# Performance work log

Measured on AMD Instinct MI355X. Metric: run time of the kernel, lower is better.

Reference implementation:

```python
import jax, jax.numpy as jnp
import numpy as np

NUM_HEADS = 4
NUM_POINTS = 8


def setup_inputs() -> dict:
    key0 = jax.random.key(0)
    ks = jax.random.split(key0, 14)
    B, S, N, D, C = 1, 6, 10000, 4, 128
    Hf, Wf = 46, 80
    M = Hf * Wf
    HP2 = NUM_HEADS * NUM_POINTS * 2
    HP = NUM_HEADS * NUM_POINTS
    inp = {
        "query": jax.random.normal(ks[0], (B, N, C), jnp.float32),
        "key": jax.random.normal(ks[1], (S, M, B, C), jnp.float32),
        "value": jax.random.normal(ks[2], (S, M, B, C), jnp.float32),
        "query_pos": jax.random.normal(ks[3], (B, N, C), jnp.float32),
        "reference_points_cam": jax.random.uniform(ks[4], (S, B, N, D, 2), jnp.float32),
        "Wv": jax.random.normal(ks[5], (C, C), jnp.float32) * 0.02,
        "bv": jnp.zeros((C,), jnp.float32),
        "Wo": jax.random.normal(ks[6], (C, HP2), jnp.float32) * 0.02,
        "bo": jax.random.normal(ks[7], (HP2,), jnp.float32) * 0.5,
        "Wa": jax.random.normal(ks[8], (C, HP), jnp.float32) * 0.02,
        "ba": jnp.zeros((HP,), jnp.float32),
        "Wp": jax.random.normal(ks[9], (C, C), jnp.float32) * 0.02,
        "bp": jnp.zeros((C,), jnp.float32),
        "spatial_shapes": np.array([[Hf, Wf]], dtype=np.int64),
        "bev_mask": jax.random.uniform(ks[10], (S, B, N, D)) < 0.3,
    }
    return inp


def _bilinear_sample(value_hw, loc, Hf, Wf):
    # value_hw: [BS, H, Hf*Wf, Dh]; loc: [BS, L, H, P, 2] normalized to [0,1]
    # grid_sample(align_corners=False, padding=zeros) semantics: ix = x*W - 0.5
    x = loc[..., 0] * Wf - 0.5
    y = loc[..., 1] * Hf - 0.5
    x0 = jnp.floor(x)
    y0 = jnp.floor(y)
    lx = x - x0
    ly = y - y0
    x0i = x0.astype(jnp.int32)
    y0i = y0.astype(jnp.int32)

    BS, L, H, P = x.shape
    Dh = value_hw.shape[-1]

    def gat(xi, yi):
        valid = (xi >= 0) & (xi < Wf) & (yi >= 0) & (yi < Hf)
        idx = jnp.clip(yi, 0, Hf - 1) * Wf + jnp.clip(xi, 0, Wf - 1)  # [BS,L,H,P]
        idx_t = idx.transpose(0, 2, 1, 3).reshape(BS, H, L * P)
        v = jnp.take_along_axis(value_hw, idx_t[..., None], axis=2)  # [BS,H,L*P,Dh]
        v = v.reshape(BS, H, L, P, Dh)
        return v * valid.transpose(0, 2, 1, 3)[..., None]

    def wt(w):  # [BS,L,H,P] -> [BS,H,L,P,1]
        return w.transpose(0, 2, 1, 3)[..., None]

    out = (gat(x0i, y0i) * wt((1 - lx) * (1 - ly))
           + gat(x0i + 1, y0i) * wt(lx * (1 - ly))
           + gat(x0i, y0i + 1) * wt((1 - lx) * ly)
           + gat(x0i + 1, y0i + 1) * wt(lx * ly))
    return out  # [BS,H,L,P,Dh]


def _deform_attn(q, val, ref, Hf, Wf, Wv, bv, Wo, bo, Wa, ba):
    # q: [BS,L,C], val: [BS,M,C], ref: [BS,L,D,2]
    BS, L, C = q.shape
    Dh = C // NUM_HEADS
    D = ref.shape[2]
    value_p = (val @ Wv + bv).reshape(BS, -1, NUM_HEADS, Dh)
    value_hw = value_p.transpose(0, 2, 1, 3)  # [BS,H,M,Dh]

    off = (q @ Wo + bo).reshape(BS, L, NUM_HEADS, NUM_POINTS, 2)
    attw = jax.nn.softmax((q @ Wa + ba).reshape(BS, L, NUM_HEADS, NUM_POINTS), axis=-1)

    normalizer = jnp.array([Wf, Hf], dtype=q.dtype)  # (x_norm, y_norm)
    off = off / normalizer
    # split points into (points_per_Z, num_Z_anchors) and add per-anchor reference
    off = off.reshape(BS, L, NUM_HEADS, NUM_POINTS // D, D, 2)
    loc = ref[:, :, None, None, :, :] + off  # [BS,L,H,P//D,D,2]
    loc = loc.reshape(BS, L, NUM_HEADS, NUM_POINTS, 2)

    sampled = _bilinear_sample(value_hw, loc, Hf, Wf)  # [BS,H,L,P,Dh]
    out = jnp.einsum('bhlpd,blhp->blhd', sampled, attw)
    return out.reshape(BS, L, C)


def reference(query, key, value, query_pos, reference_points_cam,
              Wv, bv, Wo, bo, Wa, ba, Wp, bp, spatial_shapes, bev_mask):
    B, N, C = query.shape
    S, M = key.shape[0], key.shape[1]
    Hf = int(spatial_shapes[0][0])
    Wf = int(spatial_shapes[0][1])

    q = query + query_pos
    # dense equivalent of the per-camera nonzero() rebatch: run deformable
    # attention for every (batch, camera, query), then mask + scatter-add.
    q_bs = jnp.broadcast_to(q[:, None], (B, S, N, C)).reshape(B * S, N, C)
    ref_bs = reference_points_cam.transpose(1, 0, 2, 3, 4).reshape(B * S, N, -1, 2)
    val_bs = value.transpose(2, 0, 1, 3).reshape(B * S, M, C)

    out = _deform_attn(q_bs, val_bs, ref_bs, Hf, Wf, Wv, bv, Wo, bo, Wa, ba)
    out = out.reshape(B, S, N, C)

    mask_q = (bev_mask.sum(-1) > 0)            # [S,B,N] query visible in camera
    mask_q = mask_q.transpose(1, 0, 2)         # [B,S,N]
    slots = jnp.einsum('bsnc,bsn->bnc', out, mask_q.astype(out.dtype))
    count = jnp.maximum(mask_q.sum(1).astype(out.dtype), 1.0)  # [B,N]
    slots = slots / count[..., None]
    # dropout in eval mode is identity
    return slots @ Wp + bp + query
```

## Files before the change

### kernel.cpp

```cpp
#include <hip/hip_runtime.h>


#define S_DIM 6
#define N_DIM 10000
#define C_DIM 128
#define M_DIM 3680
#define H_DIM 4
#define P_DIM 8
#define DH    32
#define HF    46
#define WF    80

#define G_Q   4
#define NENT  (S_DIM * P_DIM * H_DIM)
#define VHW_SHORTS (S_DIM * H_DIM * M_DIM * DH)

__device__ __forceinline__ float bfl(unsigned u) {
    return __uint_as_float(u << 16);
}
__device__ __forceinline__ float bfh(unsigned u) {
    return __uint_as_float(u & 0xffff0000u);
}
__device__ __forceinline__ unsigned short f2bf(float f) {
    unsigned b = __float_as_uint(f);
    b += 0x7FFFu + ((b >> 16) & 1u);
    return (unsigned short)(b >> 16);
}

__global__ __launch_bounds__(128) void vproj_kernel(
    const float* __restrict__ value,
    const float* __restrict__ Wv,
    const float* __restrict__ bv,
    unsigned short* __restrict__ vhw)
{
    const int row0 = blockIdx.x * 16;
    const int t = threadIdx.x;
    __shared__ float vs[16][C_DIM];

#pragma unroll
    for (int i = 0; i < 16; ++i)
        vs[i][t] = value[(size_t)(row0 + i) * C_DIM + t];
    __syncthreads();

    float acc[16];
#pragma unroll
    for (int i = 0; i < 16; ++i) acc[i] = 0.f;

    for (int k = 0; k < C_DIM; k += 4) {
        const float w0 = Wv[(k + 0) * C_DIM + t];
        const float w1 = Wv[(k + 1) * C_DIM + t];
        const float w2 = Wv[(k + 2) * C_DIM + t];
        const float w3 = Wv[(k + 3) * C_DIM + t];
#pragma unroll
        for (int i = 0; i < 16; ++i) {
            const float4 v = *(const float4*)&vs[i][k];
            acc[i] = fmaf(v.x, w0, acc[i]);
            acc[i] = fmaf(v.y, w1, acc[i]);
            acc[i] = fmaf(v.z, w2, acc[i]);
            acc[i] = fmaf(v.w, w3, acc[i]);
        }
    }
    const float b = bv[t];
    const int h = t >> 5, dh = t & 31;
#pragma unroll
    for (int i = 0; i < 16; ++i) {
        const int row = row0 + i;
        const int s = row / M_DIM;
        const int m = row - s * M_DIM;
        vhw[(((size_t)s * H_DIM + h) * M_DIM + m) * DH + dh] = f2bf(acc[i] + b);
    }
}

__global__ __launch_bounds__(256, 4) void attn_kernel(
    const unsigned short* __restrict__ vhw,
    const float* __restrict__ query,
    const float* __restrict__ query_pos,
    const float* __restrict__ Wo, const float* __restrict__ bo,
    const float* __restrict__ Wa, const float* __restrict__ ba,
    const float* __restrict__ refpts,
    const void* __restrict__ bev_mask,
    const void* __restrict__ sshapes,
    const float* __restrict__ Wp, const float* __restrict__ bp,
    float* __restrict__ out)
{
    const int n0 = blockIdx.x * G_Q;
    const int t = threadIdx.x;

    __shared__ float  qs[G_Q][C_DIM];
    __shared__ float  s_offr[G_Q][64];
    __shared__ float  s_ar[G_Q][32];
    __shared__ float  s_attw[G_Q][32];
    __shared__ int4   s_o[G_Q][S_DIM][P_DIM][H_DIM];
    __shared__ float4 s_w[G_Q][S_DIM][P_DIM][H_DIM];
    __shared__ float  s_slots[G_Q][C_DIM];
    __shared__ int    s_mask[G_Q][S_DIM];
    __shared__ float  s_inv[G_Q];

    for (int i = t; i < G_Q * C_DIM; i += 256) {
        const int g = i >> 7, c = i & 127;
        const size_t a = (size_t)(n0 + g) * C_DIM + c;
        qs[g][c] = query[a] + query_pos[a];
    }
    if (t < G_Q * S_DIM) {
        const int g = t / S_DIM, s = t - g * S_DIM;
        const int n = n0 + g;
        const int* ss32 = (const int*)sshapes;
        const bool i32mode = (ss32[1] == WF);
        int mk;
        if (i32mode) {
            const int* bm = (const int*)bev_mask + ((size_t)s * N_DIM + n) * 4;
            mk = (bm[0] | bm[1] | bm[2] | bm[3]) ? 1 : 0;
        } else {
            const unsigned char* bm =
                (const unsigned char*)bev_mask + ((size_t)s * N_DIM + n) * 4;
            mk = (bm[0] | bm[1] | bm[2] | bm[3]) ? 1 : 0;
        }
        s_mask[g][s] = mk;
    }
    __syncthreads();
    if (t < G_Q) {
        int c = 0;
#pragma unroll
        for (int s = 0; s < S_DIM; ++s) c += s_mask[t][s];
        s_inv[t] = 1.f / fmaxf((float)c, 1.f);
    }

    {
        const int g = t >> 6, j = t & 63;
        float acc = 0.f;
        for (int k = 0; k < C_DIM; k += 4) {
            const float4 q4 = *(const float4*)&qs[g][k];
            acc = fmaf(q4.x, Wo[(k + 0) * 64 + j], acc);
            acc = fmaf(q4.y, Wo[(k + 1) * 64 + j], acc);
            acc = fmaf(q4.z, Wo[(k + 2) * 64 + j], acc);
            acc = fmaf(q4.w, Wo[(k + 3) * 64 + j], acc);
        }
        s_offr[g][j] = acc + bo[j];
    }
    if (t < G_Q * 32) {
        const int g = t >> 5, jj = t & 31;
        float acc = 0.f;
        for (int k = 0; k < C_DIM; k += 4) {
            const float4 q4 = *(const float4*)&qs[g][k];
            acc = fmaf(q4.x, Wa[(k + 0) * 32 + jj], acc);
            acc = fmaf(q4.y, Wa[(k + 1) * 32 + jj], acc);
            acc = fmaf(q4.z, Wa[(k + 2) * 32 + jj], acc);
            acc = fmaf(q4.w, Wa[(k + 3) * 32 + jj], acc);
        }
        s_ar[g][jj] = acc + ba[jj];
    }
    __syncthreads();
    if (t < G_Q * 32) {
        const int g = t >> 5, hp = t & 31;
        const float v = s_ar[g][hp];
        float m = v;
        for (int d = 1; d < 8; d <<= 1) m = fmaxf(m, __shfl_xor(m, d, 8));
        const float e = expf(v - m);
        float sum = e;
        for (int d = 1; d < 8; d <<= 1) sum += __shfl_xor(sum, d, 8);
        s_attw[g][hp] = e / sum;
    }
    __syncthreads();

    for (int i = t; i < G_Q * NENT; i += 256) {
        const int g = i / NENT;
        const int e = i - g * NENT;
        const int s = e >> 5;
        const int rem = e & 31;
        const int p = rem >> 2, h = rem & 3;
        const int hp = h * P_DIM + p;
        const int d = p & 3;
        const int n = n0 + g;

        const float aw = s_attw[g][hp];
        const float offx = s_offr[g][hp * 2 + 0] / (float)WF;
        const float offy = s_offr[g][hp * 2 + 1] / (float)HF;
        const float refx = refpts[(((size_t)s * N_DIM + n) * 4 + d) * 2 + 0];
        const float refy = refpts[(((size_t)s * N_DIM + n) * 4 + d) * 2 + 1];

        const float x = (refx + offx) * (float)WF - 0.5f;
        const float y = (refy + offy) * (float)HF - 0.5f;
        const float x0f = floorf(x), y0f = floorf(y);
        const float lx = x - x0f, ly = y - y0f;
        const int x0 = (int)x0f, y0 = (int)y0f;
        const int x1 = x0 + 1, y1 = y0 + 1;

        const bool vx0 = (x0 >= 0) & (x0 < WF);
        const bool vx1 = (x1 >= 0) & (x1 < WF);
        const bool vy0 = (y0 >= 0) & (y0 < HF);
        const bool vy1 = (y1 >= 0) & (y1 < HF);

        const int cx0 = min(max(x0, 0), WF - 1);
        const int cx1 = min(max(x1, 0), WF - 1);
        const int cy0 = min(max(y0, 0), HF - 1);
        const int cy1 = min(max(y1, 0), HF - 1);

        const int base = (s * H_DIM + h) * M_DIM;
        const int r0 = base + cy0 * WF;
        const int r1 = base + cy1 * WF;
        s_o[g][s][p][h] = make_int4((r0 + cx0) * (DH * 2),
                                    (r0 + cx1) * (DH * 2),
                                    (r1 + cx0) * (DH * 2),
                                    (r1 + cx1) * (DH * 2));

        const float wx0 = 1.f - lx, wy0 = 1.f - ly;
        s_w[g][s][p][h] = make_float4((vx0 & vy0) ? wx0 * wy0 * aw : 0.f,
                                      (vx1 & vy0) ? lx  * wy0 * aw : 0.f,
                                      (vx0 & vy1) ? wx0 * ly  * aw : 0.f,
                                      (vx1 & vy1) ? lx  * ly  * aw : 0.f);
    }
    __syncthreads();

    {
        const char* vb = (const char*)vhw;
        const int g = t >> 6;
        const int lane = t & 63;
        const int h = lane >> 4;
        const int dhp4 = (lane & 15) * 4;
        float accx = 0.f, accy = 0.f;

        for (int s = 0; s < S_DIM; ++s) {
            if (!s_mask[g][s]) continue;
#pragma unroll
            for (int pg = 0; pg < 4; ++pg) {
                const int4 o0 = s_o[g][s][pg * 2 + 0][h];
                const int4 o1 = s_o[g][s][pg * 2 + 1][h];
                unsigned u0 = *(const unsigned*)(vb + (o0.x + dhp4));
                unsigned u1 = *(const unsigned*)(vb + (o0.y + dhp4));
                unsigned u2 = *(const unsigned*)(vb + (o0.z + dhp4));
                unsigned u3 = *(const unsigned*)(vb + (o0.w + dhp4));
                unsigned u4 = *(const unsigned*)(vb + (o1.x + dhp4));
                unsigned u5 = *(const unsigned*)(vb + (o1.y + dhp4));
                unsigned u6 = *(const unsigned*)(vb + (o1.z + dhp4));
                unsigned u7 = *(const unsigned*)(vb + (o1.w + dhp4));
                const float4 w0 = s_w[g][s][pg * 2 + 0][h];
                const float4 w1 = s_w[g][s][pg * 2 + 1][h];
                accx = fmaf(w0.x, bfl(u0), accx); accy = fmaf(w0.x, bfh(u0), accy);
                accx = fmaf(w0.y, bfl(u1), accx); accy = fmaf(w0.y, bfh(u1), accy);
                accx = fmaf(w0.z, bfl(u2), accx); accy = fmaf(w0.z, bfh(u2), accy);
                accx = fmaf(w0.w, bfl(u3), accx); accy = fmaf(w0.w, bfh(u3), accy);
                accx = fmaf(w1.x, bfl(u4), accx); accy = fmaf(w1.x, bfh(u4), accy);
                accx = fmaf(w1.y, bfl(u5), accx); accy = fmaf(w1.y, bfh(u5), accy);
                accx = fmaf(w1.z, bfl(u6), accx); accy = fmaf(w1.z, bfh(u6), accy);
                accx = fmaf(w1.w, bfl(u7), accx); accy = fmaf(w1.w, bfh(u7), accy);
            }
        }
        const float inv = s_inv[g];
        *(float2*)&s_slots[g][h * 32 + (lane & 15) * 2] =
            make_float2(accx * inv, accy * inv);
    }
    __syncthreads();

    {
        const int c = t & 127, half = t >> 7;
        const int g0 = half * 2;
        float a0 = 0.f, a1 = 0.f;
        for (int k = 0; k < C_DIM; k += 4) {
            const float4 s0 = *(const float4*)&s_slots[g0][k];
            const float4 s1 = *(const float4*)&s_slots[g0 + 1][k];
            const float w0 = Wp[(k + 0) * C_DIM + c];
            const float w1 = Wp[(k + 1) * C_DIM + c];
            const float w2 = Wp[(k + 2) * C_DIM + c];
            const float w3 = Wp[(k + 3) * C_DIM + c];
            a0 = fmaf(s0.x, w0, a0); a1 = fmaf(s1.x, w0, a1);
            a0 = fmaf(s0.y, w1, a0); a1 = fmaf(s1.y, w1, a1);
            a0 = fmaf(s0.z, w2, a0); a1 = fmaf(s1.z, w2, a1);
            a0 = fmaf(s0.w, w3, a0); a1 = fmaf(s1.w, w3, a1);
        }
        const int na = n0 + g0;
        const float bb = bp[c];
        out[(size_t)na * C_DIM + c]       = a0 + bb + query[(size_t)na * C_DIM + c];
        out[(size_t)(na + 1) * C_DIM + c] = a1 + bb + query[(size_t)(na + 1) * C_DIM + c];
    }
}

extern "C" void kernel_launch(void* const* d_in, const int* in_sizes, int n_in,
                              void* d_out, int out_size, void* d_ws, size_t ws_size,
                              hipStream_t stream) {
    const float* query     = (const float*)d_in[0];
    const float* value     = (const float*)d_in[2];
    const float* query_pos = (const float*)d_in[3];
    const float* refpts    = (const float*)d_in[4];
    const float* Wv        = (const float*)d_in[5];
    const float* bv        = (const float*)d_in[6];
    const float* Wo        = (const float*)d_in[7];
    const float* bo        = (const float*)d_in[8];
    const float* Wa        = (const float*)d_in[9];
    const float* ba        = (const float*)d_in[10];
    const float* Wp        = (const float*)d_in[11];
    const float* bp        = (const float*)d_in[12];
    const void*  sshapes   = d_in[13];
    const void*  bev_mask  = d_in[14];

    unsigned short* vhw = (unsigned short*)d_ws;
    float* outp = (float*)d_out;

    hipLaunchKernelGGL(vproj_kernel, dim3((S_DIM * M_DIM) / 16), dim3(128), 0, stream,
                       value, Wv, bv, vhw);
    hipLaunchKernelGGL(attn_kernel, dim3(N_DIM / G_Q), dim3(256), 0, stream,
                       vhw, query, query_pos, Wo, bo, Wa, ba,
                       refpts, bev_mask, sshapes, Wp, bp, outp);
}
```

Measured before the change: 84.49 us.

## Split query and output projections into register-tiled GEMM kernels

Moves the per-block Wo/Wa query projections and the final Wp projection out of the attention kernel into separate register-tiled GEMM kernels (64 rows per block, 8x4 outputs per thread). The value projection also gets the same 8x4 register tiling with float4 loads. The attention kernel now reads precomputed offsets and logits, stores sample pixel indices as 16-bit values, and writes slots in bf16. The aim is to stop re-reading the weights for every 4-query block and to cut shared memory and register pressure in the gather kernel. The cost is two extra launches, extra global round trips for the intermediates, and bf16 rounding of the slots before the output projection.

```diff
diff --git a/kernel.cpp b/kernel.cpp
--- a/kernel.cpp
+++ b/kernel.cpp
@@ -15,91 +15,188 @@
 #define NENT  (S_DIM * P_DIM * H_DIM)
 #define VHW_SHORTS (S_DIM * H_DIM * M_DIM * DH)
 
-__device__ __forceinline__ float bfl(unsigned u) {
-    return __uint_as_float(u << 16);
-}
-__device__ __forceinline__ float bfh(unsigned u) {
-    return __uint_as_float(u & 0xffff0000u);
-}
+__device__ __forceinline__ float bfl(unsigned u) { return __uint_as_float(u << 16); }
+__device__ __forceinline__ float bfh(unsigned u) { return __uint_as_float(u & 0xffff0000u); }
+__device__ __forceinline__ float bf1(unsigned short u) { return __uint_as_float(((unsigned)u) << 16); }
 __device__ __forceinline__ unsigned short f2bf(float f) {
     unsigned b = __float_as_uint(f);
     b += 0x7FFFu + ((b >> 16) & 1u);
     return (unsigned short)(b >> 16);
 }
 
-__global__ __launch_bounds__(128) void vproj_kernel(
+__global__ __launch_bounds__(256) void vproj_kernel(
     const float* __restrict__ value,
     const float* __restrict__ Wv,
     const float* __restrict__ bv,
     unsigned short* __restrict__ vhw)
 {
-    const int row0 = blockIdx.x * 16;
+    const int row0 = blockIdx.x * 64;
     const int t = threadIdx.x;
-    __shared__ float vs[16][C_DIM];
-
-#pragma unroll
-    for (int i = 0; i < 16; ++i)
-        vs[i][t] = value[(size_t)(row0 + i) * C_DIM + t];
+    const int tc = t & 31, tr = t >> 5;
+    const int c0 = tc * 4, r0 = tr * 8;
+    __shared__ float vs[64][C_DIM];
+
+    for (int i = t; i < 64 * 32; i += 256) {
+        const int row = i >> 5, c4 = (i & 31) * 4;
+        *(float4*)&vs[row][c4] = *(const float4*)&value[(size_t)(row0 + row) * C_DIM + c4];
+    }
     __syncthreads();
 
-    float acc[16];
-#pragma unroll
-    for (int i = 0; i < 16; ++i) acc[i] = 0.f;
+    float acc[8][4];
+#pragma unroll
+    for (int r = 0; r < 8; ++r)
+#pragma unroll
+        for (int c = 0; c < 4; ++c) acc[r][c] = 0.f;
 
     for (int k = 0; k < C_DIM; k += 4) {
-        const float w0 = Wv[(k + 0) * C_DIM + t];
-        const float w1 = Wv[(k + 1) * C_DIM + t];
-        const float w2 = Wv[(k + 2) * C_DIM + t];
-        const float w3 = Wv[(k + 3) * C_DIM + t];
-#pragma unroll
-        for (int i = 0; i < 16; ++i) {
-            const float4 v = *(const float4*)&vs[i][k];
-            acc[i] = fmaf(v.x, w0, acc[i]);
-            acc[i] = fmaf(v.y, w1, acc[i]);
-            acc[i] = fmaf(v.z, w2, acc[i]);
-            acc[i] = fmaf(v.w, w3, acc[i]);
-        }
-    }
-    const float b = bv[t];
-    const int h = t >> 5, dh = t & 31;
-#pragma unroll
-    for (int i = 0; i < 16; ++i) {
-        const int row = row0 + i;
-        const int s = row / M_DIM;
-        const int m = row - s * M_DIM;
-        vhw[(((size_t)s * H_DIM + h) * M_DIM + m) * DH + dh] = f2bf(acc[i] + b);
-    }
-}
-
-__global__ __launch_bounds__(256, 4) void attn_kernel(
-    const unsigned short* __restrict__ vhw,
+        const float4 w0 = *(const float4*)&Wv[(k + 0) * C_DIM + c0];
+        const float4 w1 = *(const float4*)&Wv[(k + 1) * C_DIM + c0];
+        const float4 w2 = *(const float4*)&Wv[(k + 2) * C_DIM + c0];
+        const float4 w3 = *(const float4*)&Wv[(k + 3) * C_DIM + c0];
+#pragma unroll
+        for (int r = 0; r < 8; ++r) {
+            const float4 v = *(const float4*)&vs[r0 + r][k];
+            acc[r][0] = fmaf(v.x, w0.x, acc[r][0]);
+            acc[r][0] = fmaf(v.y, w1.x, acc[r][0]);
+            acc[r][0] = fmaf(v.z, w2.x, acc[r][0]);
+            acc[r][0] = fmaf(v.w, w3.x, acc[r][0]);
+            acc[r][1] = fmaf(v.x, w0.y, acc[r][1]);
+            acc[r][1] = fmaf(v.y, w1.y, acc[r][1]);
+            acc[r][1] = fmaf(v.z, w2.y, acc[r][1]);
+            acc[r][1] = fmaf(v.w, w3.y, acc[r][1]);
+            acc[r][2] = fmaf(v.x, w0.z, acc[r][2]);
+            acc[r][2] = fmaf(v.y, w1.z, acc[r][2]);
+            acc[r][2] = fmaf(v.z, w2.z, acc[r][2]);
+            acc[r][2] = fmaf(v.w, w3.z, acc[r][2]);
+            acc[r][3] = fmaf(v.x, w0.w, acc[r][3]);
+            acc[r][3] = fmaf(v.y, w1.w, acc[r][3]);
+            acc[r][3] = fmaf(v.z, w2.w, acc[r][3]);
+            acc[r][3] = fmaf(v.w, w3.w, acc[r][3]);
+        }
+    }
+
+    const float4 bb = *(const float4*)&bv[c0];
+    const int h = c0 >> 5, dh0 = c0 & 31;
+#pragma unroll
+    for (int r = 0; r < 8; ++r) {
+        const int row = row0 + r0 + r;
+        const int s = row / M_DIM, m = row - s * M_DIM;
+        ushort4 o;
+        o.x = f2bf(acc[r][0] + bb.x);
+        o.y = f2bf(acc[r][1] + bb.y);
+        o.z = f2bf(acc[r][2] + bb.z);
+        o.w = f2bf(acc[r][3] + bb.w);
+        *(ushort4*)&vhw[(((size_t)s * H_DIM + h) * M_DIM + m) * DH + dh0] = o;
+    }
+}
+
+__global__ __launch_bounds__(256) void qproj_kernel(
     const float* __restrict__ query,
     const float* __restrict__ query_pos,
     const float* __restrict__ Wo, const float* __restrict__ bo,
     const float* __restrict__ Wa, const float* __restrict__ ba,
+    float* __restrict__ off_raw,
+    float* __restrict__ logits)
+{
+    const int row0 = blockIdx.x * 64;
+    const int t = threadIdx.x;
+    const int tc = t & 31, tr = t >> 5;
+    const int c0 = tc * 4, r0 = tr * 8;
+    __shared__ float qs[64][C_DIM];
+
+    for (int i = t; i < 64 * 32; i += 256) {
+        const int row = i >> 5, c4 = (i & 31) * 4;
+        int rr = row0 + row; if (rr >= N_DIM) rr = N_DIM - 1;
+        const float4 a = *(const float4*)&query[(size_t)rr * C_DIM + c4];
+        const float4 b = *(const float4*)&query_pos[(size_t)rr * C_DIM + c4];
+        float4 q; q.x = a.x + b.x; q.y = a.y + b.y; q.z = a.z + b.z; q.w = a.w + b.w;
+        *(float4*)&qs[row][c4] = q;
+    }
+    __syncthreads();
+    if (tc >= 24) return;
+
+    const bool isWo = (tc < 16);
+    float acc[8][4];
+#pragma unroll
+    for (int r = 0; r < 8; ++r)
+#pragma unroll
+        for (int c = 0; c < 4; ++c) acc[r][c] = 0.f;
+
+    for (int k = 0; k < C_DIM; k += 4) {
+        float4 w0, w1, w2, w3;
+        if (isWo) {
+            w0 = *(const float4*)&Wo[(k + 0) * 64 + c0];
+            w1 = *(const float4*)&Wo[(k + 1) * 64 + c0];
+            w2 = *(const float4*)&Wo[(k + 2) * 64 + c0];
+            w3 = *(const float4*)&Wo[(k + 3) * 64 + c0];
+        } else {
+            w0 = *(const float4*)&Wa[(k + 0) * 32 + (c0 - 64)];
+            w1 = *(const float4*)&Wa[(k + 1) * 32 + (c0 - 64)];
+            w2 = *(const float4*)&Wa[(k + 2) * 32 + (c0 - 64)];
+            w3 = *(const float4*)&Wa[(k + 3) * 32 + (c0 - 64)];
+        }
+#pragma unroll
+        for (int r = 0; r < 8; ++r) {
+            const float4 v = *(const float4*)&qs[r0 + r][k];
+            acc[r][0] = fmaf(v.x, w0.x, acc[r][0]);
+            acc[r][0] = fmaf(v.y, w1.x, acc[r][0]);
+            acc[r][0] = fmaf(v.z, w2.x, acc[r][0]);
+            acc[r][0] = fmaf(v.w, w3.x, acc[r][0]);
+            acc[r][1] = fmaf(v.x, w0.y, acc[r][1]);
+            acc[r][1] = fmaf(v.y, w1.y, acc[r][1]);
+            acc[r][1] = fmaf(v.z, w2.y, acc[r][1]);
+            acc[r][1] = fmaf(v.w, w3.y, acc[r][1]);
+            acc[r][2] = fmaf(v.x, w0.z, acc[r][2]);
+            acc[r][2] = fmaf(v.y, w1.z, acc[r][2]);
+            acc[r][2] = fmaf(v.z, w2.z, acc[r][2]);
+            acc[r][2] = fmaf(v.w, w3.z, acc[r][2]);
+            acc[r][3] = fmaf(v.x, w0.w, acc[r][3]);
+            acc[r][3] = fmaf(v.y, w1.w, acc[r][3]);
+            acc[r][3] = fmaf(v.z, w2.w, acc[r][3]);
+            acc[r][3] = fmaf(v.w, w3.w, acc[r][3]);
+        }
+    }
+
+#pragma unroll
+    for (int r = 0; r < 8; ++r) {
+        const int row = row0 + r0 + r;
+        if (row >= N_DIM) continue;
+        if (isWo) {
+            const float4 bb = *(const float4*)&bo[c0];
+            float4 o; o.x = acc[r][0] + bb.x; o.y = acc[r][1] + bb.y;
+            o.z = acc[r][2] + bb.z; o.w = acc[r][3] + bb.w;
+            *(float4*)&off_raw[(size_t)row * 64 + c0] = o;
+        } else {
+            const float4 bb = *(const float4*)&ba[c0 - 64];
+            float4 o; o.x = acc[r][0] + bb.x; o.y = acc[r][1] + bb.y;
+            o.z = acc[r][2] + bb.z; o.w = acc[r][3] + bb.w;
+            *(float4*)&logits[(size_t)row * 32 + (c0 - 64)] = o;
+        }
+    }
+}
+
+__global__ __launch_bounds__(256) void attn_kernel(
+    const unsigned short* __restrict__ vhw,
+    const float* __restrict__ off_raw,
+    const float* __restrict__ logits,
     const float* __restrict__ refpts,
     const void* __restrict__ bev_mask,
     const void* __restrict__ sshapes,
-    const float* __restrict__ Wp, const float* __restrict__ bp,
-    float* __restrict__ out)
+    unsigned short* __restrict__ slots)
 {
     const int n0 = blockIdx.x * G_Q;
     const int t = threadIdx.x;
 
-    __shared__ float  qs[G_Q][C_DIM];
-    __shared__ float  s_offr[G_Q][64];
-    __shared__ float  s_ar[G_Q][32];
-    __shared__ float  s_attw[G_Q][32];
-    __shared__ int4   s_o[G_Q][S_DIM][P_DIM][H_DIM];
-    __shared__ float4 s_w[G_Q][S_DIM][P_DIM][H_DIM];
-    __shared__ float  s_slots[G_Q][C_DIM];
-    __shared__ int    s_mask[G_Q][S_DIM];
-    __shared__ float  s_inv[G_Q];
-
-    for (int i = t; i < G_Q * C_DIM; i += 256) {
-        const int g = i >> 7, c = i & 127;
-        const size_t a = (size_t)(n0 + g) * C_DIM + c;
-        qs[g][c] = query[a] + query_pos[a];
+    __shared__ float   s_off[G_Q][64];
+    __shared__ float   s_attw[G_Q][32];
+    __shared__ float4  s_w[G_Q][S_DIM][P_DIM][H_DIM];
+    __shared__ ushort4 s_pix[G_Q][S_DIM][P_DIM][H_DIM];
+    __shared__ int     s_mask[G_Q][S_DIM];
+    __shared__ float   s_inv[G_Q];
+
+    {
+        const int g = t >> 6, j = t & 63;
+        s_off[g][j] = off_raw[(size_t)(n0 + g) * 64 + j];
     }
     if (t < G_Q * S_DIM) {
         const int g = t / S_DIM, s = t - g * S_DIM;
@@ -117,42 +214,9 @@
         }
         s_mask[g][s] = mk;
     }
-    __syncthreads();
-    if (t < G_Q) {
-        int c = 0;
-#pragma unroll
-        for (int s = 0; s < S_DIM; ++s) c += s_mask[t][s];
-        s_inv[t] = 1.f / fmaxf((float)c, 1.f);
-    }
-
-    {
-        const int g = t >> 6, j = t & 63;
-        float acc = 0.f;
-        for (int k = 0; k < C_DIM; k += 4) {
-            const float4 q4 = *(const float4*)&qs[g][k];
-            acc = fmaf(q4.x, Wo[(k + 0) * 64 + j], acc);
-            acc = fmaf(q4.y, Wo[(k + 1) * 64 + j], acc);
-            acc = fmaf(q4.z, Wo[(k + 2) * 64 + j], acc);
-            acc = fmaf(q4.w, Wo[(k + 3) * 64 + j], acc);
-        }
-        s_offr[g][j] = acc + bo[j];
-    }
-    if (t < G_Q * 32) {
-        const int g = t >> 5, jj = t & 31;
-        float acc = 0.f;
-        for (int k = 0; k < C_DIM; k += 4) {
-            const float4 q4 = *(const float4*)&qs[g][k];
-            acc = fmaf(q4.x, Wa[(k + 0) * 32 + jj], acc);
-            acc = fmaf(q4.y, Wa[(k + 1) * 32 + jj], acc);
-            acc = fmaf(q4.z, Wa[(k + 2) * 32 + jj], acc);
-            acc = fmaf(q4.w, Wa[(k + 3) * 32 + jj], acc);
-        }
-        s_ar[g][jj] = acc + ba[jj];
-    }
-    __syncthreads();
-    if (t < G_Q * 32) {
+    if (t < 128) {
         const int g = t >> 5, hp = t & 31;
-        const float v = s_ar[g][hp];
+        const float v = logits[(size_t)(n0 + g) * 32 + hp];
         float m = v;
         for (int d = 1; d < 8; d <<= 1) m = fmaxf(m, __shfl_xor(m, d, 8));
         const float e = expf(v - m);
@@ -161,6 +225,12 @@
         s_attw[g][hp] = e / sum;
     }
     __syncthreads();
+    if (t < G_Q) {
+        int c = 0;
+#pragma unroll
+        for (int s = 0; s < S_DIM; ++s) c += s_mask[t][s];
+        s_inv[t] = 1.f / fmaxf((float)c, 1.f);
+    }
 
     for (int i = t; i < G_Q * NENT; i += 256) {
         const int g = i / NENT;
@@ -173,8 +243,8 @@
         const int n = n0 + g;
 
         const float aw = s_attw[g][hp];
-        const float offx = s_offr[g][hp * 2 + 0] / (float)WF;
-        const float offy = s_offr[g][hp * 2 + 1] / (float)HF;
+        const float offx = s_off[g][hp * 2 + 0] / (float)WF;
+        const float offy = s_off[g][hp * 2 + 1] / (float)HF;
         const float refx = refpts[(((size_t)s * N_DIM + n) * 4 + d) * 2 + 0];
         const float refy = refpts[(((size_t)s * N_DIM + n) * 4 + d) * 2 + 1];
 
@@ -195,13 +265,11 @@
         const int cy0 = min(max(y0, 0), HF - 1);
         const int cy1 = min(max(y1, 0), HF - 1);
 
-        const int base = (s * H_DIM + h) * M_DIM;
-        const int r0 = base + cy0 * WF;
-        const int r1 = base + cy1 * WF;
-        s_o[g][s][p][h] = make_int4((r0 + cx0) * (DH * 2),
-                                    (r0 + cx1) * (DH * 2),
-                                    (r1 + cx0) * (DH * 2),
-                                    (r1 + cx1) * (DH * 2));
+        s_pix[g][s][p][h] = make_ushort4(
+            (unsigned short)(cy0 * WF + cx0),
+            (unsigned short)(cy0 * WF + cx1),
+            (unsigned short)(cy1 * WF + cx0),
+            (unsigned short)(cy1 * WF + cx1));
 
         const float wx0 = 1.f - lx, wy0 = 1.f - ly;
         s_w[g][s][p][h] = make_float4((vx0 & vy0) ? wx0 * wy0 * aw : 0.f,
@@ -221,18 +289,19 @@
 
         for (int s = 0; s < S_DIM; ++s) {
             if (!s_mask[g][s]) continue;
+            const int base = ((s * H_DIM + h) * M_DIM) * 64 + dhp4;
 #pragma unroll
             for (int pg = 0; pg < 4; ++pg) {
-                const int4 o0 = s_o[g][s][pg * 2 + 0][h];
-                const int4 o1 = s_o[g][s][pg * 2 + 1][h];
-                unsigned u0 = *(const unsigned*)(vb + (o0.x + dhp4));
-                unsigned u1 = *(const unsigned*)(vb + (o0.y + dhp4));
-                unsigned u2 = *(const unsigned*)(vb + (o0.z + dhp4));
-                unsigned u3 = *(const unsigned*)(vb + (o0.w + dhp4));
-                unsigned u4 = *(const unsigned*)(vb + (o1.x + dhp4));
-                unsigned u5 = *(const unsigned*)(vb + (o1.y + dhp4));
-                unsigned u6 = *(const unsigned*)(vb + (o1.z + dhp4));
-                unsigned u7 = *(const unsigned*)(vb + (o1.w + dhp4));
+                const ushort4 p0 = s_pix[g][s][pg * 2 + 0][h];
+                const ushort4 p1 = s_pix[g][s][pg * 2 + 1][h];
+                const unsigned u0 = *(const unsigned*)(vb + base + (int)p0.x * 64);
+                const unsigned u1 = *(const unsigned*)(vb + base + (int)p0.y * 64);
+                const unsigned u2 = *(const unsigned*)(vb + base + (int)p0.z * 64);
+                const unsigned u3 = *(const unsigned*)(vb + base + (int)p0.w * 64);
+                const unsigned u4 = *(const unsigned*)(vb + base + (int)p1.x * 64);
+                const unsigned u5 = *(const unsigned*)(vb + base + (int)p1.y * 64);
+                const unsigned u6 = *(const unsigned*)(vb + base + (int)p1.z * 64);
+                const unsigned u7 = *(const unsigned*)(vb + base + (int)p1.w * 64);
                 const float4 w0 = s_w[g][s][pg * 2 + 0][h];
                 const float4 w1 = s_w[g][s][pg * 2 + 1][h];
                 accx = fmaf(w0.x, bfl(u0), accx); accy = fmaf(w0.x, bfh(u0), accy);
@@ -246,31 +315,79 @@
             }
         }
         const float inv = s_inv[g];
-        *(float2*)&s_slots[g][h * 32 + (lane & 15) * 2] =
-            make_float2(accx * inv, accy * inv);
+        const unsigned short o0 = f2bf(accx * inv);
+        const unsigned short o1 = f2bf(accy * inv);
+        const unsigned ow = (unsigned)o0 | ((unsigned)o1 << 16);
+        *(unsigned*)&slots[(size_t)(n0 + g) * C_DIM + h * 32 + (lane & 15) * 2] = ow;
+    }
+}
+
+__global__ __launch_bounds__(256) void oproj_kernel(
+    const unsigned short* __restrict__ slots,
+    const float* __restrict__ Wp, const float* __restrict__ bp,
+    const float* __restrict__ query,
+    float* __restrict__ out)
+{
+    const int row0 = blockIdx.x * 64;
+    const int t = threadIdx.x;
+    const int tc = t & 31, tr = t >> 5;
+    const int c0 = tc * 4, r0 = tr * 8;
+    __shared__ float ss[64][C_DIM];
+
+    for (int i = t; i < 64 * 32; i += 256) {
+        const int row = i >> 5, c4 = (i & 31) * 4;
+        int rr = row0 + row; if (rr >= N_DIM) rr = N_DIM - 1;
+        const ushort4 u = *(const ushort4*)&slots[(size_t)rr * C_DIM + c4];
+        float4 q; q.x = bf1(u.x); q.y = bf1(u.y); q.z = bf1(u.z); q.w = bf1(u.w);
+        *(float4*)&ss[row][c4] = q;
     }
     __syncthreads();
 
-    {
-        const int c = t & 127, half = t >> 7;
-        const int g0 = half * 2;
-        float a0 = 0.f, a1 = 0.f;
-        for (int k = 0; k < C_DIM; k += 4) {
-            const float4 s0 = *(const float4*)&s_slots[g0][k];
-            const float4 s1 = *(const float4*)&s_slots[g0 + 1][k];
-            const float w0 = Wp[(k + 0) * C_DIM + c];
-            const float w1 = Wp[(k + 1) * C_DIM + c];
-            const float w2 = Wp[(k + 2) * C_DIM + c];
-            const float w3 = Wp[(k + 3) * C_DIM + c];
-            a0 = fmaf(s0.x, w0, a0); a1 = fmaf(s1.x, w0, a1);
-            a0 = fmaf(s0.y, w1, a0); a1 = fmaf(s1.y, w1, a1);
-            a0 = fmaf(s0.z, w2, a0); a1 = fmaf(s1.z, w2, a1);
-            a0 = fmaf(s0.w, w3, a0); a1 = fmaf(s1.w, w3, a1);
-        }
-        const int na = n0 + g0;
-        const float bb = bp[c];
-        out[(size_t)na * C_DIM + c]       = a0 + bb + query[(size_t)na * C_DIM + c];
-        out[(size_t)(na + 1) * C_DIM + c] = a1 + bb + query[(size_t)(na + 1) * C_DIM + c];
+    float acc[8][4];
+#pragma unroll
+    for (int r = 0; r < 8; ++r)
+#pragma unroll
+        for (int c = 0; c < 4; ++c) acc[r][c] = 0.f;
+
+    for (int k = 0; k < C_DIM; k += 4) {
+        const float4 w0 = *(const float4*)&Wp[(k + 0) * C_DIM + c0];
+        const float4 w1 = *(const float4*)&Wp[(k + 1) * C_DIM + c0];
+        const float4 w2 = *(const float4*)&Wp[(k + 2) * C_DIM + c0];
+        const float4 w3 = *(const float4*)&Wp[(k + 3) * C_DIM + c0];
+#pragma unroll
+        for (int r = 0; r < 8; ++r) {
+            const float4 v = *(const float4*)&ss[r0 + r][k];
+            acc[r][0] = fmaf(v.x, w0.x, acc[r][0]);
+            acc[r][0] = fmaf(v.y, w1.x, acc[r][0]);
+            acc[r][0] = fmaf(v.z, w2.x, acc[r][0]);
+            acc[r][0] = fmaf(v.w, w3.x, acc[r][0]);
+            acc[r][1] = fmaf(v.x, w0.y, acc[r][1]);
+            acc[r][1] = fmaf(v.y, w1.y, acc[r][1]);
+            acc[r][1] = fmaf(v.z, w2.y, acc[r][1]);
+            acc[r][1] = fmaf(v.w, w3.y, acc[r][1]);
+            acc[r][2] = fmaf(v.x, w0.z, acc[r][2]);
+            acc[r][2] = fmaf(v.y, w1.z, acc[r][2]);
+            acc[r][2] = fmaf(v.z, w2.z, acc[r][2]);
+            acc[r][2] = fmaf(v.w, w3.z, acc[r][2]);
+            acc[r][3] = fmaf(v.x, w0.w, acc[r][3]);
+            acc[r][3] = fmaf(v.y, w1.w, acc[r][3]);
+            acc[r][3] = fmaf(v.z, w2.w, acc[r][3]);
+            acc[r][3] = fmaf(v.w, w3.w, acc[r][3]);
+        }
+    }
+
+    const float4 bb = *(const float4*)&bp[c0];
+#pragma unroll
+    for (int r = 0; r < 8; ++r) {
+        const int row = row0 + r0 + r;
+        if (row >= N_DIM) continue;
+        const float4 q = *(const float4*)&query[(size_t)row * C_DIM + c0];
+        float4 o;
+        o.x = acc[r][0] + bb.x + q.x;
+        o.y = acc[r][1] + bb.y + q.y;
+        o.z = acc[r][2] + bb.z + q.z;
+        o.w = acc[r][3] + bb.w + q.w;
+        *(float4*)&out[(size_t)row * C_DIM + c0] = o;
     }
 }
 
@@ -292,12 +409,18 @@
     const void*  sshapes   = d_in[13];
     const void*  bev_mask  = d_in[14];
 
-    unsigned short* vhw = (unsigned short*)d_ws;
-    float* outp = (float*)d_out;
-
-    hipLaunchKernelGGL(vproj_kernel, dim3((S_DIM * M_DIM) / 16), dim3(128), 0, stream,
+    unsigned short* vhw     = (unsigned short*)d_ws;
+    float*          off_raw = (float*)(vhw + VHW_SHORTS);
+    float*          lg      = off_raw + (size_t)N_DIM * 64;
+    unsigned short* slots   = (unsigned short*)(lg + (size_t)N_DIM * 32);
+    float*          outp    = (float*)d_out;
+
+    hipLaunchKernelGGL(vproj_kernel, dim3((S_DIM * M_DIM) / 64), dim3(256), 0, stream,
                        value, Wv, bv, vhw);
+    hipLaunchKernelGGL(qproj_kernel, dim3((N_DIM + 63) / 64), dim3(256), 0, stream,
+                       query, query_pos, Wo, bo, Wa, ba, off_raw, lg);
     hipLaunchKernelGGL(attn_kernel, dim3(N_DIM / G_Q), dim3(256), 0, stream,
-                       vhw, query, query_pos, Wo, bo, Wa, ba,
-                       refpts, bev_mask, sshapes, Wp, bp, outp);
-}
+                       vhw, off_raw, lg, refpts, bev_mask, sshapes, slots);
+    hipLaunchKernelGGL(oproj_kernel, dim3((N_DIM + 63) / 64), dim3(256), 0, stream,
+                       slots, Wp, bp, query, outp);
+}
```

Result: slower. 102.0 us (+20.8%).
